# Optimization experiments

Hardware: AMD Instinct MI355X
Metric: run time of the kernel (lower is better)

The kernel has to match this reference:

```python
import jax, jax.numpy as jnp
import numpy as np

T, D, I, E, TOPK = 4096, 1024, 1024, 8, 2

def setup_inputs() -> dict:
    key = jax.random.key(0)
    ks = jax.random.split(key, 5)
    scale = 1.0 / np.sqrt(D)
    return {
        "x": jax.random.normal(ks[0], (T, D), dtype=jnp.float32),
        "gate_w": jax.random.normal(ks[1], (E, D), dtype=jnp.float32) * scale,
        "w1": jax.random.normal(ks[2], (E, I, D), dtype=jnp.float32) * scale,
        "w3": jax.random.normal(ks[3], (E, I, D), dtype=jnp.float32) * scale,
        "w2": jax.random.normal(ks[4], (E, D, I), dtype=jnp.float32) * (1.0 / np.sqrt(I)),
    }

def reference(x, gate_w, w1, w3, w2):
    # Gate: softmax over experts, then top-k (weights are pre-top-k softmax probs)
    scores = jax.nn.softmax(x @ gate_w.T, axis=-1)          # [T, E]
    weights, indices = jax.lax.top_k(scores, TOPK)          # [T, K], [T, K]

    # Dense SwiGLU for every expert over all tokens (faithful to masked loop:
    # experts are bias-free so expert(x*mask) == mask * expert(x))
    h = jnp.einsum('td,eid->eti', x, w1)                    # [E, T, I]
    g = jnp.einsum('td,eid->eti', x, w3)                    # [E, T, I]
    a = jax.nn.silu(h) * g                                  # [E, T, I]
    out = jnp.einsum('eti,edi->etd', a, w2)                 # [E, T, D]

    # Gather each token's top-k expert outputs and combine with routing weights
    out_t = jnp.transpose(out, (1, 0, 2))                   # [T, E, D]
    sel = jnp.take_along_axis(out_t, indices[:, :, None], axis=1)  # [T, K, D]
    y = jnp.sum(sel * weights[:, :, None], axis=1)          # [T, D]
    return y
```

## Files before the change

kernel.cpp:

```cpp
#include <hip/hip_runtime.h>
#include <hip/hip_bf16.h>

typedef unsigned short u16;
typedef unsigned int u32;
typedef __attribute__((ext_vector_type(8))) short bf16x8;
typedef __attribute__((ext_vector_type(4))) float f32x4;

#define NEXP 8
#define NTOK 4096
#define DDIM 1024
#define MAX_TILES 80

__device__ __forceinline__ u16 f2bf(float f) {
    u32 u = __float_as_uint(f);
    u += 0x7fff + ((u >> 16) & 1);
    return (u16)(u >> 16);
}

__device__ __forceinline__ void gload16(const void* g, void* l) {
    __builtin_amdgcn_global_load_lds((const __attribute__((address_space(1))) u32*)g,
                                     (__attribute__((address_space(3))) u32*)l, 16, 0, 0);
}

__device__ __forceinline__ void cvt8(const float* src, u16* dst) {
    float4 a = ((const float4*)src)[0], b = ((const float4*)src)[1];
    uint4 o;
    o.x = (u32)f2bf(a.x) | ((u32)f2bf(a.y) << 16);
    o.y = (u32)f2bf(a.z) | ((u32)f2bf(a.w) << 16);
    o.z = (u32)f2bf(b.x) | ((u32)f2bf(b.y) << 16);
    o.w = (u32)f2bf(b.z) | ((u32)f2bf(b.w) << 16);
    *(uint4*)dst = o;
}

__global__ __launch_bounds__(256) void gate_cvt_kernel(const float* __restrict__ x,
                                                       const float* __restrict__ gw,
                                                       const float* __restrict__ w1,
                                                       const float* __restrict__ w3,
                                                       int* __restrict__ t2i, float* __restrict__ t2w,
                                                       u16* __restrict__ xb, u16* __restrict__ wb) {
    int bid = blockIdx.x;
    int tid = threadIdx.x;
    if (bid >= 1024) {
        for (int i = (bid - 1024) * 256 + tid; i < 2097152; i += 131072) {
            const float* src = (i < 1048576) ? w1 + (size_t)i * 8 : w3 + ((size_t)i - 1048576) * 8;
            cvt8(src, wb + (size_t)i * 8);
        }
        return;
    }
    int wv = tid >> 6, lane = tid & 63;
    int t = bid * 4 + wv;
    const float4* xr = (const float4*)(x + (size_t)t * DDIM);
    float4 xv[4];
#pragma unroll
    for (int q = 0; q < 4; q++) xv[q] = xr[lane * 4 + q];

    uint4 o0, o1;
    o0.x = (u32)f2bf(xv[0].x) | ((u32)f2bf(xv[0].y) << 16);
    o0.y = (u32)f2bf(xv[0].z) | ((u32)f2bf(xv[0].w) << 16);
    o0.z = (u32)f2bf(xv[1].x) | ((u32)f2bf(xv[1].y) << 16);
    o0.w = (u32)f2bf(xv[1].z) | ((u32)f2bf(xv[1].w) << 16);
    o1.x = (u32)f2bf(xv[2].x) | ((u32)f2bf(xv[2].y) << 16);
    o1.y = (u32)f2bf(xv[2].z) | ((u32)f2bf(xv[2].w) << 16);
    o1.z = (u32)f2bf(xv[3].x) | ((u32)f2bf(xv[3].y) << 16);
    o1.w = (u32)f2bf(xv[3].z) | ((u32)f2bf(xv[3].w) << 16);
    uint4* xbo = (uint4*)(xb + (size_t)t * DDIM + lane * 16);
    xbo[0] = o0;
    xbo[1] = o1;

    float acc[NEXP];
#pragma unroll
    for (int e = 0; e < NEXP; e++) acc[e] = 0.f;
#pragma unroll
    for (int e = 0; e < NEXP; e++) {
#pragma unroll
        for (int q = 0; q < 4; q++) {
            float4 g = ((const float4*)gw)[e * 256 + lane * 4 + q];
            acc[e] += xv[q].x * g.x + xv[q].y * g.y + xv[q].z * g.z + xv[q].w * g.w;
        }
    }
#pragma unroll
    for (int e = 0; e < NEXP; e++) {
        float v = acc[e];
#pragma unroll
        for (int off = 32; off; off >>= 1) v += __shfl_xor(v, off, 64);
        acc[e] = v;
    }
    if (lane == 0) {
        float m = acc[0];
#pragma unroll
        for (int e = 1; e < NEXP; e++) m = fmaxf(m, acc[e]);
        float p[NEXP]; float s = 0.f;
#pragma unroll
        for (int e = 0; e < NEXP; e++) { p[e] = __expf(acc[e] - m); s += p[e]; }
        float inv = 1.f / s;
        float best = -1.f, sec = -1.f; int bi = 0, si = 0;
#pragma unroll
        for (int e = 0; e < NEXP; e++) {
            float pe = p[e] * inv;
            if (pe > best) { sec = best; si = bi; best = pe; bi = e; }
            else if (pe > sec) { sec = pe; si = e; }
        }
        t2i[2 * t] = bi;  t2i[2 * t + 1] = si;
        t2w[2 * t] = best; t2w[2 * t + 1] = sec;
    }
}

__global__ __launch_bounds__(1024) void sort_kernel(const int* __restrict__ t2i,
                                                    const float* __restrict__ t2w,
                                                    int* __restrict__ ctl,
                                                    int* __restrict__ slot_token,
                                                    float* __restrict__ slot_wt,
                                                    int* __restrict__ t2slot) {
    __shared__ int sb[NEXP][1024];
    __shared__ int wsum[16];
    __shared__ int sex[16];
    __shared__ int stot[NEXP];
    __shared__ int soffs[NEXP + 1];
    int tid = threadIdx.x;
    int lane = tid & 63, wv = tid >> 6;

    int4 a = *(const int4*)(t2i + tid * 8);
    int4 b = *(const int4*)(t2i + tid * 8 + 4);
    int ev0 = a.x, ev1 = a.y, ev2 = a.z, ev3 = a.w;
    int ev4 = b.x, ev5 = b.y, ev6 = b.z, ev7 = b.w;
    u32 cnt = (1u << (ev0 * 4)) + (1u << (ev1 * 4)) + (1u << (ev2 * 4)) + (1u << (ev3 * 4)) +
              (1u << (ev4 * 4)) + (1u << (ev5 * 4)) + (1u << (ev6 * 4)) + (1u << (ev7 * 4));

    for (int e = 0; e < NEXP; e++) {
        int v = (cnt >> (e * 4)) & 15;
        int inc = v;
#pragma unroll
        for (int off = 1; off < 64; off <<= 1) {
            int n = __shfl_up(inc, off, 64);
            if (lane >= off) inc += n;
        }
        if (lane == 63) wsum[wv] = inc;
        __syncthreads();
        if (wv == 0) {
            int w = (lane < 16) ? wsum[lane] : 0;
            int winc = w;
#pragma unroll
            for (int off = 1; off < 16; off <<= 1) {
                int n = __shfl_up(winc, off, 64);
                if (lane >= off) winc += n;
            }
            if (lane < 16) sex[lane] = winc - w;
            if (lane == 15) stot[e] = winc;
        }
        __syncthreads();
        sb[e][tid] = sex[wv] + inc - v;
        __syncthreads();
    }
    if (tid == 0) {
        int o = 0, tt = 0;
        for (int e = 0; e < NEXP; e++) {
            soffs[e] = o;
            ctl[16 + e] = o;
            ctl[280 + e] = tt;
            int n = stot[e];
            for (int r = 0; r < n; r += 128) {
                ctl[32 + tt] = e; ctl[112 + tt] = o + r; ctl[192 + tt] = o + n; tt++;
            }
            o += n;
        }
        soffs[NEXP] = o; ctl[24] = o; ctl[25] = tt; ctl[288] = tt;
    }
    __syncthreads();
#pragma unroll
    for (int j = 0; j < 8; j++) {
        int e;
        switch (j) {
            case 0: e = ev0; break; case 1: e = ev1; break; case 2: e = ev2; break;
            case 3: e = ev3; break; case 4: e = ev4; break; case 5: e = ev5; break;
            case 6: e = ev6; break; default: e = ev7; break;
        }
        int base = sb[e][tid];
        sb[e][tid] = base + 1;
        int slot = soffs[e] + base;
        int p = tid * 8 + j;
        slot_token[slot] = p >> 1;
        slot_wt[slot] = t2w[p];
        t2slot[p] = slot;
    }
}

__global__ __launch_bounds__(256, 4) void gemm0_kernel(
    const u16* __restrict__ Amat, const u16* __restrict__ B1g, const u16* __restrict__ B2g,
    const float* __restrict__ w2, u16* __restrict__ w2b,
    u16* __restrict__ OutB,
    const int* __restrict__ ctl, const int* __restrict__ slot_token) {
    constexpr int NB = 2;
    constexpr int NCB = 16;
    constexpr int NK = 32;

    int bid = blockIdx.x;
    if (bid < 512) {
        int tid0 = bid * 256 + threadIdx.x;
        for (int i = tid0; i < 1048576; i += 131072)
            cvt8(w2 + (size_t)i * 8, w2b + (size_t)i * 8);
        return;
    }
    bid -= 512;
    int ntiles = ctl[25];
    int N = ntiles * NCB;
    if (bid >= N) return;
    int q = N >> 3, r = N & 7;
    int xcd = bid & 7, seq = bid >> 3;
    int n = (xcd < r ? xcd * (q + 1) : r * (q + 1) + (xcd - r) * q) + seq;
    int e = 0, tstart = 0, tiles_e = 0, m = n;
    for (; e < NEXP; e++) {
        tstart = ctl[280 + e];
        tiles_e = ctl[281 + e] - tstart;
        int sz = tiles_e * NCB;
        if (m < sz) break;
        m -= sz;
    }
    if (e == NEXP) return;
    int cb = m / tiles_e;
    int tt = tstart + (m - cb * tiles_e);
    int rowbase = ctl[112 + tt];
    int segend = ctl[192 + tt];

    __shared__ __align__(16) u16 smem[2 * 128 * 32 + 2 * 64 * 32 + 2 * 64 * 32];
    u16* sA = smem;
    u16* sB1 = smem + 2 * 128 * 32;
    u16* sB2 = sB1 + 2 * 64 * 32;

    int tid = threadIdx.x;
    int lane = tid & 63;
    int wv = tid >> 6;
    int wrow = wv >> 1, wcol = wv & 1;
    int lr = lane >> 2;
    int cS = (((lane & 3) ^ ((lane >> 3) & 3)) << 3);
    int l15 = lane & 15, hi = lane >> 4;
    int csr = ((hi ^ ((l15 >> 1) & 3)) << 3);

    u32 rowA[2];
#pragma unroll
    for (int i = 0; i < 2; i++) {
        int slot = rowbase + wv * 32 + i * 16 + lr;
        if (slot >= segend) slot = rowbase;
        rowA[i] = (u32)slot_token[slot] * 1024;
    }
    u32 rowB0;
    {
        int rr = cb * 64 + wv * 16 + lr;
        rowB0 = (u32)e * 1048576 + (u32)rr * 1024;
    }

    f32x4 accH[4][NB], accG[4][NB];
    f32x4 zero = {0.f, 0.f, 0.f, 0.f};
#pragma unroll
    for (int m2 = 0; m2 < 4; m2++)
#pragma unroll
        for (int nn = 0; nn < NB; nn++) { accH[m2][nn] = zero; accG[m2][nn] = zero; }

    auto stage = [&](int buf, int kt) {
        int k0 = kt * 32 + cS;
        gload16(Amat + rowA[0] + k0, sA + buf * 4096 + (wv * 32) * 32);
        gload16(Amat + rowA[1] + k0, sA + buf * 4096 + (wv * 32 + 16) * 32);
        gload16(B1g + rowB0 + k0, sB1 + buf * 2048 + (wv * 16) * 32);
        gload16(B2g + rowB0 + k0, sB2 + buf * 2048 + (wv * 16) * 32);
    };

    auto compute = [&](int buf) {
        bf16x8 av[4];
#pragma unroll
        for (int m2 = 0; m2 < 4; m2++) {
            int rr = wrow * 64 + m2 * 16 + l15;
            av[m2] = *(const bf16x8*)(sA + buf * 4096 + rr * 32 + csr);
        }
        bf16x8 b1v[NB], b2v[NB];
#pragma unroll
        for (int nn = 0; nn < NB; nn++) {
            int rr = wcol * 32 + nn * 16 + l15;
            b1v[nn] = *(const bf16x8*)(sB1 + buf * 2048 + rr * 32 + csr);
            b2v[nn] = *(const bf16x8*)(sB2 + buf * 2048 + rr * 32 + csr);
        }
#pragma unroll
        for (int m2 = 0; m2 < 4; m2++)
#pragma unroll
            for (int nn = 0; nn < NB; nn++) {
                accH[m2][nn] = __builtin_amdgcn_mfma_f32_16x16x32_bf16(av[m2], b1v[nn], accH[m2][nn], 0, 0, 0);
                accG[m2][nn] = __builtin_amdgcn_mfma_f32_16x16x32_bf16(av[m2], b2v[nn], accG[m2][nn], 0, 0, 0);
            }
    };

    stage(0, 0);
    for (int kt = 0; kt < NK; ++kt) {
        __syncthreads();
        if (kt + 1 < NK) stage((kt + 1) & 1, kt + 1);
        compute(kt & 1);
    }

    int colblock = cb * 64 + wcol * 32;
#pragma unroll
    for (int m2 = 0; m2 < 4; m2++) {
        int slotbase = rowbase + wrow * 64 + m2 * 16 + hi * 4;
#pragma unroll
        for (int nn = 0; nn < NB; nn++) {
            int col = colblock + nn * 16 + l15;
#pragma unroll
            for (int j = 0; j < 4; j++) {
                int slot = slotbase + j;
                if (slot < segend) {
                    float h = accH[m2][nn][j], g = accG[m2][nn][j];
                    float aa = (h / (1.f + __expf(-h))) * g;
                    OutB[(size_t)slot * 1024 + col] = f2bf(aa);
                }
            }
        }
    }
}

__global__ __launch_bounds__(256, 4) void gemm1_kernel(
    const u16* __restrict__ Abuf, const u16* __restrict__ w2b, float* __restrict__ Y2,
    const int* __restrict__ ctl) {
    constexpr int NCB = 8;
    constexpr int NK = 32;

    int ntiles = ctl[25];
    int N = ntiles * NCB;
    int bid = blockIdx.x;
    if (bid >= N) return;
    int q = N >> 3, r = N & 7;
    int xcd = bid & 7, seq = bid >> 3;
    int n = (xcd < r ? xcd * (q + 1) : r * (q + 1) + (xcd - r) * q) + seq;
    int e = 0, tstart = 0, tiles_e = 0, m = n;
    for (; e < NEXP; e++) {
        tstart = ctl[280 + e];
        tiles_e = ctl[281 + e] - tstart;
        int sz = tiles_e * NCB;
        if (m < sz) break;
        m -= sz;
    }
    if (e == NEXP) return;
    int cb = m / tiles_e;
    int tt = tstart + (m - cb * tiles_e);
    int rowbase = ctl[112 + tt];
    int segend = ctl[192 + tt];

    __shared__ __align__(16) u16 smem[2 * 128 * 32 * 2];
    u16* sA = smem;
    u16* sB = smem + 2 * 128 * 32;

    int tid = threadIdx.x;
    int lane = tid & 63;
    int wv = tid >> 6;
    int wrow = wv >> 1, wcol = wv & 1;
    int lr = lane >> 2;
    int cS = (((lane & 3) ^ ((lane >> 3) & 3)) << 3);
    int l15 = lane & 15, hi = lane >> 4;
    int csr = ((hi ^ ((l15 >> 1) & 3)) << 3);

    u32 rowA[2], rowB[2];
#pragma unroll
    for (int i = 0; i < 2; i++) {
        int slot = rowbase + wv * 32 + i * 16 + lr;
        if (slot >= segend) slot = rowbase;
        rowA[i] = (u32)slot * 1024;
        int rr = cb * 128 + wv * 32 + i * 16 + lr;
        rowB[i] = (u32)e * 1048576 + (u32)rr * 1024;
    }

    f32x4 acc[4][4];
    f32x4 zero = {0.f, 0.f, 0.f, 0.f};
#pragma unroll
    for (int m2 = 0; m2 < 4; m2++)
#pragma unroll
        for (int nn = 0; nn < 4; nn++) acc[m2][nn] = zero;

    auto stage = [&](int buf, int kt) {
        int k0 = kt * 32 + cS;
#pragma unroll
        for (int i = 0; i < 2; i++) {
            gload16(Abuf + rowA[i] + k0, sA + buf * 4096 + (wv * 32 + i * 16) * 32);
            gload16(w2b + rowB[i] + k0, sB + buf * 4096 + (wv * 32 + i * 16) * 32);
        }
    };

    auto compute = [&](int buf) {
        bf16x8 av[4], bv[4];
#pragma unroll
        for (int m2 = 0; m2 < 4; m2++) {
            int rr = wrow * 64 + m2 * 16 + l15;
            av[m2] = *(const bf16x8*)(sA + buf * 4096 + rr * 32 + csr);
        }
#pragma unroll
        for (int nn = 0; nn < 4; nn++) {
            int rr = wcol * 64 + nn * 16 + l15;
            bv[nn] = *(const bf16x8*)(sB + buf * 4096 + rr * 32 + csr);
        }
#pragma unroll
        for (int m2 = 0; m2 < 4; m2++)
#pragma unroll
            for (int nn = 0; nn < 4; nn++)
                acc[m2][nn] = __builtin_amdgcn_mfma_f32_16x16x32_bf16(av[m2], bv[nn], acc[m2][nn], 0, 0, 0);
    };

    stage(0, 0);
    for (int kt = 0; kt < NK; ++kt) {
        __syncthreads();
        if (kt + 1 < NK) stage((kt + 1) & 1, kt + 1);
        compute(kt & 1);
    }

    int colblock = cb * 128 + wcol * 64;
#pragma unroll
    for (int m2 = 0; m2 < 4; m2++) {
        int slotbase = rowbase + wrow * 64 + m2 * 16 + hi * 4;
#pragma unroll
        for (int nn = 0; nn < 4; nn++) {
            int col = colblock + nn * 16 + l15;
#pragma unroll
            for (int j = 0; j < 4; j++) {
                int slot = slotbase + j;
                if (slot < segend)
                    Y2[(size_t)slot * 1024 + col] = acc[m2][nn][j];
            }
        }
    }
}

__global__ __launch_bounds__(256) void combine_kernel(const float* __restrict__ Y2,
                                                      const int* __restrict__ t2slot,
                                                      const float* __restrict__ t2w,
                                                      float* __restrict__ y) {
    int t = blockIdx.x;
    int d = threadIdx.x * 4;
    int s0 = t2slot[2 * t], s1 = t2slot[2 * t + 1];
    float w0 = t2w[2 * t], w1 = t2w[2 * t + 1];
    float4 a = *(const float4*)(Y2 + (size_t)s0 * 1024 + d);
    float4 b = *(const float4*)(Y2 + (size_t)s1 * 1024 + d);
    float4 o;
    o.x = w0 * a.x + w1 * b.x;
    o.y = w0 * a.y + w1 * b.y;
    o.z = w0 * a.z + w1 * b.z;
    o.w = w0 * a.w + w1 * b.w;
    *(float4*)(y + (size_t)t * 1024 + d) = o;
}

extern "C" void kernel_launch(void* const* d_in, const int* in_sizes, int n_in,
                              void* d_out, int out_size, void* d_ws, size_t ws_size,
                              hipStream_t stream) {
    const float* x  = (const float*)d_in[0];
    const float* gw = (const float*)d_in[1];
    const float* w1 = (const float*)d_in[2];
    const float* w3 = (const float*)d_in[3];
    const float* w2 = (const float*)d_in[4];
    float* y = (float*)d_out;
    char* ws = (char*)d_ws;

    int*   ctl        = (int*)ws;
    int*   t2i        = (int*)(ws + 4096);
    float* t2w        = (float*)(ws + 36864);
    int*   slot_token = (int*)(ws + 69632);
    float* slot_wt    = (float*)(ws + 102400);
    int*   t2slot     = (int*)(ws + 135168);
    u16*   xb   = (u16*)(ws + 262144);
    u16*   w1b  = xb  + (size_t)4194304;
    u16*   w3b  = w1b + (size_t)8388608;
    u16*   w2b  = w3b + (size_t)8388608;
    u16*   Abuf = w2b + (size_t)8388608;
    float* Y2 = (float*)w1b;

    gate_cvt_kernel<<<1536, 256, 0, stream>>>(x, gw, w1, w3, t2i, t2w, xb, w1b);
    sort_kernel<<<1, 1024, 0, stream>>>(t2i, t2w, ctl, slot_token, slot_wt, t2slot);

    gemm0_kernel<<<512 + MAX_TILES * 16, 256, 0, stream>>>(
        xb, w1b, w3b, w2, w2b, Abuf, ctl, slot_token);
    gemm1_kernel<<<MAX_TILES * 8, 256, 0, stream>>>(Abuf, w2b, Y2, ctl);
    combine_kernel<<<NTOK, 256, 0, stream>>>(Y2, t2slot, t2w, y);
}
```

Baseline: 137.1 us.

## Move w2 bf16 conversion into gate kernel and store expert outputs as bf16

The w2 fp32-to-bf16 conversion moves out of the gemm0 prologue blocks and into the gate/convert kernel's conversion loop, which now covers w1, w3 and w2 contiguously. gemm1 writes its per-slot outputs as bf16 instead of fp32, and the combine kernel reads and widens them, halving intermediate write and read traffic. gemm0's occupancy hint is raised from 4 to 5 blocks per SM. The trade-offs are extra bf16 rounding of expert outputs before combining, possible register pressure from the occupancy bound, and a longer gate/convert kernel.

New measurement: 142.6 us. 1.04x slower.

```diff
diff --git a/kernel.cpp b/kernel.cpp
--- a/kernel.cpp
+++ b/kernel.cpp
@@ -16,6 +16,8 @@
     u += 0x7fff + ((u >> 16) & 1);
     return (u16)(u >> 16);
 }
+
+__device__ __forceinline__ float bf2f(u32 u) { return __uint_as_float(u << 16); }
 
 __device__ __forceinline__ void gload16(const void* g, void* l) {
     __builtin_amdgcn_global_load_lds((const __attribute__((address_space(1))) u32*)g,
@@ -36,13 +38,17 @@
                                                        const float* __restrict__ gw,
                                                        const float* __restrict__ w1,
                                                        const float* __restrict__ w3,
+                                                       const float* __restrict__ w2,
                                                        int* __restrict__ t2i, float* __restrict__ t2w,
                                                        u16* __restrict__ xb, u16* __restrict__ wb) {
     int bid = blockIdx.x;
     int tid = threadIdx.x;
     if (bid >= 1024) {
-        for (int i = (bid - 1024) * 256 + tid; i < 2097152; i += 131072) {
-            const float* src = (i < 1048576) ? w1 + (size_t)i * 8 : w3 + ((size_t)i - 1048576) * 8;
+        for (int i = (bid - 1024) * 256 + tid; i < 3145728; i += 131072) {
+            const float* src;
+            if (i < 1048576)       src = w1 + (size_t)i * 8;
+            else if (i < 2097152)  src = w3 + ((size_t)i - 1048576) * 8;
+            else                   src = w2 + ((size_t)i - 2097152) * 8;
             cvt8(src, wb + (size_t)i * 8);
         }
         return;
@@ -184,9 +190,8 @@
     }
 }
 
-__global__ __launch_bounds__(256, 4) void gemm0_kernel(
+__global__ __launch_bounds__(256, 5) void gemm0_kernel(
     const u16* __restrict__ Amat, const u16* __restrict__ B1g, const u16* __restrict__ B2g,
-    const float* __restrict__ w2, u16* __restrict__ w2b,
     u16* __restrict__ OutB,
     const int* __restrict__ ctl, const int* __restrict__ slot_token) {
     constexpr int NB = 2;
@@ -194,13 +199,6 @@
     constexpr int NK = 32;
 
     int bid = blockIdx.x;
-    if (bid < 512) {
-        int tid0 = bid * 256 + threadIdx.x;
-        for (int i = tid0; i < 1048576; i += 131072)
-            cvt8(w2 + (size_t)i * 8, w2b + (size_t)i * 8);
-        return;
-    }
-    bid -= 512;
     int ntiles = ctl[25];
     int N = ntiles * NCB;
     if (bid >= N) return;
@@ -314,7 +312,7 @@
 }
 
 __global__ __launch_bounds__(256, 4) void gemm1_kernel(
-    const u16* __restrict__ Abuf, const u16* __restrict__ w2b, float* __restrict__ Y2,
+    const u16* __restrict__ Abuf, const u16* __restrict__ w2b, u16* __restrict__ Y2,
     const int* __restrict__ ctl) {
     constexpr int NCB = 8;
     constexpr int NK = 32;
@@ -416,13 +414,13 @@
             for (int j = 0; j < 4; j++) {
                 int slot = slotbase + j;
                 if (slot < segend)
-                    Y2[(size_t)slot * 1024 + col] = acc[m2][nn][j];
+                    Y2[(size_t)slot * 1024 + col] = f2bf(acc[m2][nn][j]);
             }
         }
     }
 }
 
-__global__ __launch_bounds__(256) void combine_kernel(const float* __restrict__ Y2,
+__global__ __launch_bounds__(256) void combine_kernel(const u16* __restrict__ Y2,
                                                       const int* __restrict__ t2slot,
                                                       const float* __restrict__ t2w,
                                                       float* __restrict__ y) {
@@ -430,13 +428,13 @@
     int d = threadIdx.x * 4;
     int s0 = t2slot[2 * t], s1 = t2slot[2 * t + 1];
     float w0 = t2w[2 * t], w1 = t2w[2 * t + 1];
-    float4 a = *(const float4*)(Y2 + (size_t)s0 * 1024 + d);
-    float4 b = *(const float4*)(Y2 + (size_t)s1 * 1024 + d);
+    uint2 a = *(const uint2*)(Y2 + (size_t)s0 * 1024 + d);
+    uint2 b = *(const uint2*)(Y2 + (size_t)s1 * 1024 + d);
     float4 o;
-    o.x = w0 * a.x + w1 * b.x;
-    o.y = w0 * a.y + w1 * b.y;
-    o.z = w0 * a.z + w1 * b.z;
-    o.w = w0 * a.w + w1 * b.w;
+    o.x = w0 * bf2f(a.x & 0xffffu) + w1 * bf2f(b.x & 0xffffu);
+    o.y = w0 * bf2f(a.x >> 16)     + w1 * bf2f(b.x >> 16);
+    o.z = w0 * bf2f(a.y & 0xffffu) + w1 * bf2f(b.y & 0xffffu);
+    o.w = w0 * bf2f(a.y >> 16)     + w1 * bf2f(b.y >> 16);
     *(float4*)(y + (size_t)t * 1024 + d) = o;
 }
 
@@ -462,13 +460,13 @@
     u16*   w3b  = w1b + (size_t)8388608;
     u16*   w2b  = w3b + (size_t)8388608;
     u16*   Abuf = w2b + (size_t)8388608;
-    float* Y2 = (float*)w1b;
-
-    gate_cvt_kernel<<<1536, 256, 0, stream>>>(x, gw, w1, w3, t2i, t2w, xb, w1b);
+    u16* Y2 = w1b;
+
+    gate_cvt_kernel<<<1536, 256, 0, stream>>>(x, gw, w1, w3, w2, t2i, t2w, xb, w1b);
     sort_kernel<<<1, 1024, 0, stream>>>(t2i, t2w, ctl, slot_token, slot_wt, t2slot);
 
-    gemm0_kernel<<<512 + MAX_TILES * 16, 256, 0, stream>>>(
-        xb, w1b, w3b, w2, w2b, Abuf, ctl, slot_token);
+    gemm0_kernel<<<MAX_TILES * 16, 256, 0, stream>>>(
+        xb, w1b, w3b, Abuf, ctl, slot_token);
     gemm1_kernel<<<MAX_TILES * 8, 256, 0, stream>>>(Abuf, w2b, Y2, ctl);
     combine_kernel<<<NTOK, 256, 0, stream>>>(Y2, t2slot, t2w, y);
 }
```
